# Kernel tuning notes

Hardware: AMD Instinct MI355X
Metric: run time of the kernel (lower is better)

The kernel has to match this reference:

```python
import jax, jax.numpy as jnp
import numpy as np

ALPHA, GAMMA, EPS = 0.25, 2.0, 1e-8
COST_CLASS, COST_BBOX, COST_GIOU = 2.0, 5.0, 2.0


def box_cxcywh_to_xyxy(b):
    cx, cy, w, h = jnp.split(b, 4, axis=-1)
    return jnp.concatenate([cx - 0.5 * w, cy - 0.5 * h, cx + 0.5 * w, cy + 0.5 * h], axis=-1)


def setup_inputs() -> dict:
    key = jax.random.key(0)
    k1, k2, k3, k4 = jax.random.split(key, 4)
    bs, Q, C, T = 16, 900, 80, 1600
    return {
        "pred_logits": jax.random.normal(k1, (bs, Q, C), jnp.float32),
        "pred_boxes": jax.random.uniform(k2, (bs, Q, 4), jnp.float32),
        "tgt_labels": jax.random.randint(k3, (T,), 0, C),
        "tgt_boxes": jax.random.uniform(k4, (T, 4), jnp.float32),
        "g_size": 3,
    }


def reference(pred_logits, pred_boxes, tgt_labels, tgt_boxes, g_size):
    bs, Q, _ = pred_logits.shape
    # focal classification cost (use_focal=True path)
    p = jax.nn.sigmoid(pred_logits.reshape(bs * Q, -1))  # [N, C]
    neg = (1.0 - ALPHA) * p ** GAMMA * (-jnp.log(1.0 - p + EPS))
    pos = ALPHA * (1.0 - p) ** GAMMA * (-jnp.log(p + EPS))
    cost_class = (pos - neg)[:, tgt_labels]  # [N, T]
    # L1 box cost (cdist p=1)
    out_bbox = pred_boxes.reshape(bs * Q, 4)
    cost_bbox = jnp.abs(out_bbox[:, None, :] - tgt_bbox_b(tgt_boxes)).sum(-1)  # [N, T]
    # GIoU cost
    b1 = box_cxcywh_to_xyxy(out_bbox)  # [N, 4]
    b2 = box_cxcywh_to_xyxy(tgt_boxes)  # [T, 4]
    area1 = (b1[:, 2] - b1[:, 0]) * (b1[:, 3] - b1[:, 1])
    area2 = (b2[:, 2] - b2[:, 0]) * (b2[:, 3] - b2[:, 1])
    lt = jnp.maximum(b1[:, None, :2], b2[None, :, :2])
    rb = jnp.minimum(b1[:, None, 2:], b2[None, :, 2:])
    wh = jnp.clip(rb - lt, 0.0)
    inter = wh[..., 0] * wh[..., 1]
    union = area1[:, None] + area2[None, :] - inter
    iou = inter / union
    elt = jnp.minimum(b1[:, None, :2], b2[None, :, :2])
    erb = jnp.maximum(b1[:, None, 2:], b2[None, :, 2:])
    ewh = jnp.clip(erb - elt, 0.0)
    earea = ewh[..., 0] * ewh[..., 1]
    giou = iou - (earea - union) / earea
    # weighted total cost, then group reduction (note: original names it Cmin but takes max over the group dim)
    Cmat = COST_BBOX * cost_bbox + COST_CLASS * cost_class + COST_GIOU * (-giou)
    Cmin = Cmat.reshape(bs, Q // g_size, g_size, -1).max(axis=2)  # [bs, Q//g, T]
    return Cmin


def tgt_bbox_b(tgt_boxes):
    return tgt_boxes[None, :, :]
```

## Files before the change

### kernel.cpp

```cpp
#include <hip/hip_runtime.h>

#define ALPHA 0.25f
#define EPS   1e-8f

constexpr int BS     = 16;
constexpr int QN     = 900;
constexpr int CN     = 80;
constexpr int GS     = 3;
constexpr int WAVES  = 4;
constexpr int NT     = WAVES * 64;
constexpr int ROWS   = WAVES * GS;
constexpr int TSPLIT = 2;

__global__ __launch_bounds__(NT) void fused_cost_kernel(
    const float* __restrict__ pred_logits,
    const float* __restrict__ pred_boxes,
    const int*   __restrict__ tgt_labels,
    const float* __restrict__ tgt_boxes,
    float*       __restrict__ out,
    int T)
{
    __shared__ float s_cc[ROWS * CN];

    const int tid  = threadIdx.x;
    const int wv   = tid >> 6;
    const int lane = tid & 63;
    const int b    = blockIdx.z;
    const int n0   = b * QN + blockIdx.y * ROWS;

    const float* lg0 = pred_logits + (size_t)n0 * CN;
    #pragma unroll
    for (int k = tid; k < ROWS * CN; k += NT) {
        float x = lg0[k];
        float p = __fdividef(1.0f, 1.0f + __expf(-x));
        float omp = 1.0f - p;
        float pos = ALPHA * omp * omp * (-__logf(p + EPS));
        float neg = (1.0f - ALPHA) * p * p * (-__logf(omp + EPS));
        s_cc[k] = 2.0f * (pos - neg) + 2.0f;
    }

    float Pcx[GS], Pcy[GS], Pw[GS], Ph[GS];
    float Px0[GS], Py0[GS], Px1[GS], Py1[GS], Pa[GS];
    #pragma unroll
    for (int g = 0; g < GS; ++g) {
        const float4 pb = ((const float4*)pred_boxes)[n0 + wv * GS + g];
        Pcx[g] = pb.x;  Pcy[g] = pb.y;  Pw[g] = pb.z;  Ph[g] = pb.w;
        Px0[g] = pb.x - 0.5f * pb.z;  Py0[g] = pb.y - 0.5f * pb.w;
        Px1[g] = pb.x + 0.5f * pb.z;  Py1[g] = pb.y + 0.5f * pb.w;
        Pa[g]  = pb.z * pb.w;
    }
    __syncthreads();

    const int qg = blockIdx.y * WAVES + wv;
    float* __restrict__ outp = out + (size_t)(b * (QN / GS) + qg) * T;
    const int ccRow = (wv * GS) * CN;

    const int tChunk = T / TSPLIT;
    const int t0     = blockIdx.x * tChunk;
    const int nFull  = tChunk >> 6;
    const int tail   = tChunk & 63;

    auto body = [&](int t) {
        const float4 tr = ((const float4*)tgt_boxes)[t];
        const int lab   = tgt_labels[t];
        const float tx0 = tr.x - 0.5f * tr.z, ty0 = tr.y - 0.5f * tr.w;
        const float tx1 = tr.x + 0.5f * tr.z, ty1 = tr.y + 0.5f * tr.w;
        const float ta  = tr.z * tr.w;

        float ccs[GS];
        #pragma unroll
        for (int g = 0; g < GS; ++g) ccs[g] = s_cc[ccRow + g * CN + lab];

        float m = -3.402823466e+38f;
        #pragma unroll
        for (int g = 0; g < GS; ++g) {
            float l1 = fabsf(Pcx[g] - tr.x) + fabsf(Pcy[g] - tr.y)
                     + fabsf(Pw[g]  - tr.z) + fabsf(Ph[g]  - tr.w);

            float iw = fminf(Px1[g], tx1) - fmaxf(Px0[g], tx0);
            float ih = fminf(Py1[g], ty1) - fmaxf(Py0[g], ty0);
            float inter = fmaxf(iw, 0.0f) * fmaxf(ih, 0.0f);
            float uni   = Pa[g] + ta - inter;

            float ew = fmaxf(Px1[g], tx1) - fminf(Px0[g], tx0);
            float eh = fmaxf(Py1[g], ty1) - fminf(Py0[g], ty0);
            float earea = ew * eh;

            float num = fmaf(inter, earea, uni * uni);
            float q   = __fdividef(num, uni * earea);

            float cost = fmaf(5.0f, l1, fmaf(-2.0f, q, ccs[g]));
            m = fmaxf(m, cost);
        }
        outp[t] = m;
    };

    #pragma unroll 2
    for (int i = 0; i < nFull; ++i)
        body(t0 + (i << 6) + lane);
    if (lane < tail)
        body(t0 + (nFull << 6) + lane);
}

extern "C" void kernel_launch(void* const* d_in, const int* in_sizes, int n_in,
                              void* d_out, int out_size, void* d_ws, size_t ws_size,
                              hipStream_t stream) {
    const float* pred_logits = (const float*)d_in[0];
    const float* pred_boxes  = (const float*)d_in[1];
    const int*   tgt_labels  = (const int*)d_in[2];
    const float* tgt_boxes   = (const float*)d_in[3];

    const int T = in_sizes[2];
    float* out = (float*)d_out;

    dim3 grid(TSPLIT, (QN / GS) / WAVES, BS);
    fused_cost_kernel<<<grid, NT, 0, stream>>>(
        pred_logits, pred_boxes, tgt_labels, tgt_boxes, out, T);
}
```

Before: 102.7 us.

## Batch target loads per pass and drop target-split grid dimension

Each block now covers all targets instead of splitting T across two blocks, and the wave count per block drops from 4 to 2. Each pass loads five targets' boxes, labels and class costs up front, then computes them, to raise memory-level parallelism per thread. This avoids recomputing the per-row logit transform in two blocks, at the cost of a longer serial loop per block. The pass count is T/(64*5), so there is no tail handling and it is only correct when T is a multiple of 320 (1600 is).

```diff
diff --git a/kernel.cpp b/kernel.cpp
--- a/kernel.cpp
+++ b/kernel.cpp
@@ -7,10 +7,10 @@
 constexpr int QN     = 900;
 constexpr int CN     = 80;
 constexpr int GS     = 3;
-constexpr int WAVES  = 4;
+constexpr int WAVES  = 2;
 constexpr int NT     = WAVES * 64;
 constexpr int ROWS   = WAVES * GS;
-constexpr int TSPLIT = 2;
+constexpr int TBATCH = 5;
 
 __global__ __launch_bounds__(NT) void fused_cost_kernel(
     const float* __restrict__ pred_logits,
@@ -25,11 +25,10 @@
     const int tid  = threadIdx.x;
     const int wv   = tid >> 6;
     const int lane = tid & 63;
-    const int b    = blockIdx.z;
-    const int n0   = b * QN + blockIdx.y * ROWS;
+    const int b    = blockIdx.y;
+    const int n0   = b * QN + blockIdx.x * ROWS;
 
     const float* lg0 = pred_logits + (size_t)n0 * CN;
-    #pragma unroll
     for (int k = tid; k < ROWS * CN; k += NT) {
         float x = lg0[k];
         float p = __fdividef(1.0f, 1.0f + __expf(-x));
@@ -51,55 +50,60 @@
     }
     __syncthreads();
 
-    const int qg = blockIdx.y * WAVES + wv;
+    const int qg = blockIdx.x * WAVES + wv;
     float* __restrict__ outp = out + (size_t)(b * (QN / GS) + qg) * T;
     const int ccRow = (wv * GS) * CN;
 
-    const int tChunk = T / TSPLIT;
-    const int t0     = blockIdx.x * tChunk;
-    const int nFull  = tChunk >> 6;
-    const int tail   = tChunk & 63;
+    const int nPass = T / (64 * TBATCH);
 
-    auto body = [&](int t) {
-        const float4 tr = ((const float4*)tgt_boxes)[t];
-        const int lab   = tgt_labels[t];
-        const float tx0 = tr.x - 0.5f * tr.z, ty0 = tr.y - 0.5f * tr.w;
-        const float tx1 = tr.x + 0.5f * tr.z, ty1 = tr.y + 0.5f * tr.w;
-        const float ta  = tr.z * tr.w;
+    for (int p = 0; p < nPass; ++p) {
+        float4 tr[TBATCH];
+        int    lab[TBATCH];
+        int    tIdx[TBATCH];
+        #pragma unroll
+        for (int j = 0; j < TBATCH; ++j) {
+            tIdx[j] = (p * TBATCH + j) * 64 + lane;
+            tr[j]   = ((const float4*)tgt_boxes)[tIdx[j]];
+            lab[j]  = tgt_labels[tIdx[j]];
+        }
+        float ccs[TBATCH][GS];
+        #pragma unroll
+        for (int j = 0; j < TBATCH; ++j)
+            #pragma unroll
+            for (int g = 0; g < GS; ++g)
+                ccs[j][g] = s_cc[ccRow + g * CN + lab[j]];
 
-        float ccs[GS];
         #pragma unroll
-        for (int g = 0; g < GS; ++g) ccs[g] = s_cc[ccRow + g * CN + lab];
+        for (int j = 0; j < TBATCH; ++j) {
+            const float tcx = tr[j].x, tcy = tr[j].y, tw = tr[j].z, th = tr[j].w;
+            const float tx0 = tcx - 0.5f * tw, ty0 = tcy - 0.5f * th;
+            const float tx1 = tcx + 0.5f * tw, ty1 = tcy + 0.5f * th;
+            const float ta  = tw * th;
 
-        float m = -3.402823466e+38f;
-        #pragma unroll
-        for (int g = 0; g < GS; ++g) {
-            float l1 = fabsf(Pcx[g] - tr.x) + fabsf(Pcy[g] - tr.y)
-                     + fabsf(Pw[g]  - tr.z) + fabsf(Ph[g]  - tr.w);
+            float m = -3.402823466e+38f;
+            #pragma unroll
+            for (int g = 0; g < GS; ++g) {
+                float l1 = fabsf(Pcx[g] - tcx) + fabsf(Pcy[g] - tcy)
+                         + fabsf(Pw[g]  - tw)  + fabsf(Ph[g]  - th);
 
-            float iw = fminf(Px1[g], tx1) - fmaxf(Px0[g], tx0);
-            float ih = fminf(Py1[g], ty1) - fmaxf(Py0[g], ty0);
-            float inter = fmaxf(iw, 0.0f) * fmaxf(ih, 0.0f);
-            float uni   = Pa[g] + ta - inter;
+                float iw = fminf(Px1[g], tx1) - fmaxf(Px0[g], tx0);
+                float ih = fminf(Py1[g], ty1) - fmaxf(Py0[g], ty0);
+                float inter = fmaxf(iw, 0.0f) * fmaxf(ih, 0.0f);
+                float uni   = Pa[g] + ta - inter;
 
-            float ew = fmaxf(Px1[g], tx1) - fminf(Px0[g], tx0);
-            float eh = fmaxf(Py1[g], ty1) - fminf(Py0[g], ty0);
-            float earea = ew * eh;
+                float ew = fmaxf(Px1[g], tx1) - fminf(Px0[g], tx0);
+                float eh = fmaxf(Py1[g], ty1) - fminf(Py0[g], ty0);
+                float earea = ew * eh;
 
-            float num = fmaf(inter, earea, uni * uni);
-            float q   = __fdividef(num, uni * earea);
+                float num = fmaf(inter, earea, uni * uni);
+                float q   = __fdividef(num, uni * earea);
 
-            float cost = fmaf(5.0f, l1, fmaf(-2.0f, q, ccs[g]));
-            m = fmaxf(m, cost);
+                float cost = fmaf(5.0f, l1, fmaf(-2.0f, q, ccs[j][g]));
+                m = fmaxf(m, cost);
+            }
+            outp[tIdx[j]] = m;
         }
-        outp[t] = m;
-    };
-
-    #pragma unroll 2
-    for (int i = 0; i < nFull; ++i)
-        body(t0 + (i << 6) + lane);
-    if (lane < tail)
-        body(t0 + (nFull << 6) + lane);
+    }
 }
 
 extern "C" void kernel_launch(void* const* d_in, const int* in_sizes, int n_in,
@@ -113,7 +117,7 @@
     const int T = in_sizes[2];
     float* out = (float*)d_out;
 
-    dim3 grid(TSPLIT, (QN / GS) / WAVES, BS);
+    dim3 grid((QN / GS) / WAVES, BS);
     fused_cost_kernel<<<grid, NT, 0, stream>>>(
         pred_logits, pred_boxes, tgt_labels, tgt_boxes, out, T);
 }
```

Measured after the change: 106.9 us. 4.1% more time.
